# Kernel optimization log

Measured on AMD Instinct MI355X. Metric: run time of the kernel, lower is better.

Reference implementation:

```python
import jax, jax.numpy as jnp
import numpy as np

N_NODES = 50000


def setup_inputs() -> dict:
    key = jax.random.key(0)
    k1, k2, k3, k4 = jax.random.split(key, 4)
    in_c, out_c = 128, 128
    x = jax.random.normal(k1, (N_NODES, in_c), dtype=jnp.float32)
    edge_index = jax.random.randint(k2, (2, 600000), 0, N_NODES, dtype=jnp.int64)
    W_l = jax.random.normal(k3, (out_c, in_c), dtype=jnp.float32) / np.sqrt(in_c)
    W_r = jax.random.normal(k4, (out_c, in_c), dtype=jnp.float32) / np.sqrt(in_c)
    b = jnp.zeros((out_c,), dtype=jnp.float32)
    return {"x": x, "edge_index": edge_index, "W_l": W_l, "W_r": W_r, "b": b}


def reference(x, edge_index, W_l, W_r, b):
    # SAGEConv (PyG defaults): mean aggregation over incoming neighbors,
    # out = lin_l(mean_agg) + lin_r(x) + bias, then log_softmax over features.
    src, dst = edge_index[0], edge_index[1]
    msgs = x[src]  # [E, in_c] gather of source features
    summed = jax.ops.segment_sum(msgs, dst, num_segments=N_NODES)  # [N, in_c]
    counts = jax.ops.segment_sum(jnp.ones_like(dst, dtype=x.dtype), dst,
                                 num_segments=N_NODES)  # [N]
    agg = summed / jnp.maximum(counts, 1.0)[:, None]  # mean; 0 for isolated nodes
    out = agg @ W_l.T + x @ W_r.T + b  # [N, out_c]
    return jax.nn.log_softmax(out, axis=1)
```

## Files before the change

### kernel.cpp

```cpp
#include <hip/hip_runtime.h>
#include <cmath>

#define C    128
#define PAD  64
#define NXCD 8

typedef __bf16 bf16x8 __attribute__((ext_vector_type(8)));
typedef float  f32x4  __attribute__((ext_vector_type(4)));
typedef unsigned short u16x8 __attribute__((ext_vector_type(8)));

static __device__ __forceinline__ unsigned short f2b(float f) {
    unsigned int u = __builtin_bit_cast(unsigned int, f);
    u += 0x7FFFu + ((u >> 16) & 1u);
    return (unsigned short)(u >> 16);
}
static __device__ __forceinline__ float b2f(unsigned short u) {
    return __builtin_bit_cast(float, (unsigned int)u << 16);
}

__global__ __launch_bounds__(256)
void sage_init(const float* __restrict__ Wl, const float* __restrict__ Wr,
               int4* __restrict__ counts4, unsigned short* __restrict__ wp,
               int n4, int ZB) {
    int bid = blockIdx.x;
    int t = threadIdx.x;
    if (bid < ZB) {
        int i = bid * 256 + t;
        if (i < n4) counts4[i] = make_int4(0, 0, 0, 0);
    } else {
        int s = (bid - ZB) * 256 + t;
        int f = s >> 6, l = s & 63;
        int kt = f >> 4, mt = f & 15;
        int g = l >> 4;
        int m = mt * 16 + (l & 15);
        const float* src = (m < C) ? (Wl + (size_t)m * C)
                                   : (Wr + (size_t)(m - C) * C);
        u16x8 o;
#pragma unroll
        for (int j = 0; j < 8; ++j) o[j] = f2b(src[kt * 32 + g * 8 + j]);
        *(u16x8*)(wp + (size_t)s * 8) = o;
    }
}

__global__ __launch_bounds__(256)
void sage_fill_gemm(const float* __restrict__ x,
                    const unsigned short* __restrict__ wp,
                    const float* __restrict__ bias,
                    const int* __restrict__ ei,
                    int* __restrict__ counts, unsigned short* __restrict__ csr,
                    unsigned short* __restrict__ yl,
                    unsigned short* __restrict__ yr,
                    int N, int E, int FB) {
    int bid = blockIdx.x;
    int t = threadIdx.x;

    if (bid < FB) {
        int xcd = bid & (NXCD - 1);
        int chunk = bid >> 3;
        int span = (N + NXCD - 1) / NXCD;
        int lo = xcd * span;
        int hi = min(N, lo + span);
        int e0 = (chunk * 256 + t) * 8;
        if (e0 + 7 < E) {
            int4 d0 = *(const int4*)(ei + E + e0);
            int4 d1 = *(const int4*)(ei + E + e0 + 4);
            int4 s0 = *(const int4*)(ei + e0);
            int4 s1 = *(const int4*)(ei + e0 + 4);
            int dd[8] = {d0.x, d0.y, d0.z, d0.w, d1.x, d1.y, d1.z, d1.w};
            int ss[8] = {s0.x, s0.y, s0.z, s0.w, s1.x, s1.y, s1.z, s1.w};
#pragma unroll
            for (int j = 0; j < 8; ++j) {
                if (dd[j] >= lo && dd[j] < hi) {
                    int k = atomicAdd(&counts[dd[j]], 1);
                    if (k < PAD)
                        csr[(size_t)dd[j] * PAD + k] = (unsigned short)ss[j];
                }
            }
        } else {
            for (int e = e0; e < E; ++e) {
                int dst = ei[E + e];
                if (dst >= lo && dst < hi) {
                    int k = atomicAdd(&counts[dst], 1);
                    if (k < PAD)
                        csr[(size_t)dst * PAD + k] = (unsigned short)ei[e];
                }
            }
        }
        return;
    }

    int w = t >> 6, l = t & 63;
    int g = l >> 4;

    int node = (bid - FB) * 16 + (l & 15);
    if (node >= N) node = N - 1;
    const float4* xv = (const float4*)(x + (size_t)node * C);
    const bf16x8* A = (const bf16x8*)wp;

    f32x4 acc0 = {0.f,0.f,0.f,0.f}, acc1 = {0.f,0.f,0.f,0.f};
    f32x4 acc2 = {0.f,0.f,0.f,0.f}, acc3 = {0.f,0.f,0.f,0.f};

#pragma unroll
    for (int kt = 0; kt < 4; ++kt) {
        float4 xa = xv[kt * 8 + g * 2];
        float4 xc = xv[kt * 8 + g * 2 + 1];
        u16x8 ab;
        ab[0]=f2b(xa.x); ab[1]=f2b(xa.y); ab[2]=f2b(xa.z); ab[3]=f2b(xa.w);
        ab[4]=f2b(xc.x); ab[5]=f2b(xc.y); ab[6]=f2b(xc.z); ab[7]=f2b(xc.w);
        bf16x8 xf = __builtin_bit_cast(bf16x8, ab);
        int c = w * 4;
        bf16x8 a0 = A[(size_t)(kt * 16 + c + 0) * 64 + l];
        bf16x8 a1 = A[(size_t)(kt * 16 + c + 1) * 64 + l];
        bf16x8 a2 = A[(size_t)(kt * 16 + c + 2) * 64 + l];
        bf16x8 a3 = A[(size_t)(kt * 16 + c + 3) * 64 + l];
        acc0 = __builtin_amdgcn_mfma_f32_16x16x32_bf16(a0, xf, acc0, 0,0,0);
        acc1 = __builtin_amdgcn_mfma_f32_16x16x32_bf16(a1, xf, acc1, 0,0,0);
        acc2 = __builtin_amdgcn_mfma_f32_16x16x32_bf16(a2, xf, acc2, 0,0,0);
        acc3 = __builtin_amdgcn_mfma_f32_16x16x32_bf16(a3, xf, acc3, 0,0,0);
    }

    size_t rowoff = (size_t)node * C;
#pragma unroll
    for (int i = 0; i < 4; ++i) {
        f32x4 a = (i == 0) ? acc0 : (i == 1) ? acc1 : (i == 2) ? acc2 : acc3;
        int mt = w * 4 + i;
        float4 bv = (mt >= 8) ? *(const float4*)(bias + (mt - 8) * 16 + g * 4)
                              : make_float4(0.f, 0.f, 0.f, 0.f);
        ushort4 o;
        o.x = f2b(a[0] + bv.x);
        o.y = f2b(a[1] + bv.y);
        o.z = f2b(a[2] + bv.z);
        o.w = f2b(a[3] + bv.w);
        unsigned short* yp = (mt < 8) ? yl : yr;
        *(ushort4*)(yp + rowoff + (mt & 7) * 16 + g * 4) = o;
    }
}

__global__ __launch_bounds__(256)
void sage_final(const unsigned short* __restrict__ yl,
                const unsigned short* __restrict__ yr,
                const int* __restrict__ counts,
                const unsigned short* __restrict__ csr,
                float* __restrict__ out, int N) {
    int wv = threadIdx.x >> 6;
    int node = blockIdx.x * 4 + wv;
    if (node >= N) return;
    int ln = threadIdx.x & 63;
    int q = ln >> 4;
    int fl = ln & 15;

    int deg = counts[node];
    deg = (deg > PAD) ? PAD : deg;
    int p0 = node * PAD;
    int p1 = p0 + deg;

    float a[8];
#pragma unroll
    for (int j = 0; j < 8; ++j) a[j] = 0.f;

    int p = p0 + q;
    for (; p + 12 < p1; p += 16) {
        int s0 = csr[p], s1 = csr[p + 4], s2 = csr[p + 8], s3 = csr[p + 12];
        u16x8 v0 = *(const u16x8*)(yl + (size_t)s0 * C + fl * 8);
        u16x8 v1 = *(const u16x8*)(yl + (size_t)s1 * C + fl * 8);
        u16x8 v2 = *(const u16x8*)(yl + (size_t)s2 * C + fl * 8);
        u16x8 v3 = *(const u16x8*)(yl + (size_t)s3 * C + fl * 8);
#pragma unroll
        for (int j = 0; j < 8; ++j)
            a[j] += (b2f(v0[j]) + b2f(v1[j])) + (b2f(v2[j]) + b2f(v3[j]));
    }
    for (; p + 4 < p1; p += 8) {
        int s0 = csr[p], s1 = csr[p + 4];
        u16x8 v0 = *(const u16x8*)(yl + (size_t)s0 * C + fl * 8);
        u16x8 v1 = *(const u16x8*)(yl + (size_t)s1 * C + fl * 8);
#pragma unroll
        for (int j = 0; j < 8; ++j) a[j] += b2f(v0[j]) + b2f(v1[j]);
    }
    if (p < p1) {
        int s0 = csr[p];
        u16x8 v0 = *(const u16x8*)(yl + (size_t)s0 * C + fl * 8);
#pragma unroll
        for (int j = 0; j < 8; ++j) a[j] += b2f(v0[j]);
    }

#pragma unroll
    for (int j = 0; j < 8; ++j) {
        a[j] += __shfl_xor(a[j], 16);
        a[j] += __shfl_xor(a[j], 32);
    }
    if (q != 0) return;

    float inv = 1.0f / fmaxf((float)deg, 1.0f);
    u16x8 yv = *(const u16x8*)(yr + (size_t)node * C + fl * 8);
#pragma unroll
    for (int j = 0; j < 8; ++j) a[j] = a[j] * inv + b2f(yv[j]);

    float m = a[0];
#pragma unroll
    for (int j = 1; j < 8; ++j) m = fmaxf(m, a[j]);
#pragma unroll
    for (int off = 1; off < 16; off <<= 1)
        m = fmaxf(m, __shfl_xor(m, off));
    float s = 0.f;
#pragma unroll
    for (int j = 0; j < 8; ++j) s += expf(a[j] - m);
#pragma unroll
    for (int off = 1; off < 16; off <<= 1)
        s += __shfl_xor(s, off);
    float ls = m + logf(s);

    float4 o0, o1;
    o0.x = a[0] - ls; o0.y = a[1] - ls; o0.z = a[2] - ls; o0.w = a[3] - ls;
    o1.x = a[4] - ls; o1.y = a[5] - ls; o1.z = a[6] - ls; o1.w = a[7] - ls;
    float4* op = (float4*)(out + (size_t)node * C + fl * 8);
    op[0] = o0;
    op[1] = o1;
}

extern "C" void kernel_launch(void* const* d_in, const int* in_sizes, int n_in,
                              void* d_out, int out_size, void* d_ws, size_t ws_size,
                              hipStream_t stream) {
    const float* x  = (const float*)d_in[0];
    const int*   ei = (const int*)d_in[1];
    const float* Wl = (const float*)d_in[2];
    const float* Wr = (const float*)d_in[3];
    const float* b  = (const float*)d_in[4];
    float* out = (float*)d_out;

    const int N = in_sizes[0] / C;
    const int E = in_sizes[1] / 2;

    int* counts = (int*)d_ws;
    unsigned short* csr = (unsigned short*)(counts + ((N + 3) & ~3));
    unsigned short* yl  = csr + (size_t)N * PAD;
    unsigned short* yr  = yl + (size_t)N * C;
    unsigned short* wp  = yr + (size_t)N * C;

    int n4 = (N + 3) / 4;
    const int ZB = (n4 + 255) / 256;
    const int NCH = (E + 2047) / 2048;
    const int FB = NCH * NXCD;
    const int NT = (N + 15) / 16;

    sage_init<<<ZB + 16, 256, 0, stream>>>(Wl, Wr, (int4*)counts, wp, n4, ZB);
    sage_fill_gemm<<<FB + NT, 256, 0, stream>>>(x, wp, b, ei, counts, csr,
                                                yl, yr, N, E, FB);
    sage_final<<<(N + 3) / 4, 256, 0, stream>>>(yl, yr, counts, csr, out, N);
}
```

Baseline: 97.84 us.

## Interleave fill and GEMM blocks and keep weight fragments across four tiles

The fused fill/GEMM kernel now interleaves three edge-fill blocks with one GEMM block in each group of four, so the scatter and the matrix work share the GPU at the same time instead of running as two separate block ranges. Each GEMM block loads its weight fragments and bias into registers once and reuses them across four 16-node tiles, cutting repeated weight loads and the number of GEMM blocks. This raises register use per thread and serialises four tiles inside one block, which may reduce latency hiding.

```diff
diff --git a/kernel.cpp b/kernel.cpp
--- a/kernel.cpp
+++ b/kernel.cpp
@@ -50,13 +50,17 @@
                     int* __restrict__ counts, unsigned short* __restrict__ csr,
                     unsigned short* __restrict__ yl,
                     unsigned short* __restrict__ yr,
-                    int N, int E, int FB) {
+                    int N, int E, int FB, int NT) {
     int bid = blockIdx.x;
     int t = threadIdx.x;
-
-    if (bid < FB) {
-        int xcd = bid & (NXCD - 1);
-        int chunk = bid >> 3;
+    int grp = bid >> 2;
+    int pos = bid & 3;
+
+    if (pos < 3) {
+        int idx = grp * 3 + pos;
+        if (idx >= FB) return;
+        int xcd = idx & (NXCD - 1);
+        int chunk = idx >> 3;
         int span = (N + NXCD - 1) / NXCD;
         int lo = xcd * span;
         int hi = min(N, lo + span);
@@ -91,48 +95,62 @@
 
     int w = t >> 6, l = t & 63;
     int g = l >> 4;
-
-    int node = (bid - FB) * 16 + (l & 15);
-    if (node >= N) node = N - 1;
-    const float4* xv = (const float4*)(x + (size_t)node * C);
     const bf16x8* A = (const bf16x8*)wp;
 
-    f32x4 acc0 = {0.f,0.f,0.f,0.f}, acc1 = {0.f,0.f,0.f,0.f};
-    f32x4 acc2 = {0.f,0.f,0.f,0.f}, acc3 = {0.f,0.f,0.f,0.f};
-
+    bf16x8 wf0[4], wf1[4], wf2[4], wf3[4];
 #pragma unroll
     for (int kt = 0; kt < 4; ++kt) {
-        float4 xa = xv[kt * 8 + g * 2];
-        float4 xc = xv[kt * 8 + g * 2 + 1];
-        u16x8 ab;
-        ab[0]=f2b(xa.x); ab[1]=f2b(xa.y); ab[2]=f2b(xa.z); ab[3]=f2b(xa.w);
-        ab[4]=f2b(xc.x); ab[5]=f2b(xc.y); ab[6]=f2b(xc.z); ab[7]=f2b(xc.w);
-        bf16x8 xf = __builtin_bit_cast(bf16x8, ab);
-        int c = w * 4;
-        bf16x8 a0 = A[(size_t)(kt * 16 + c + 0) * 64 + l];
-        bf16x8 a1 = A[(size_t)(kt * 16 + c + 1) * 64 + l];
-        bf16x8 a2 = A[(size_t)(kt * 16 + c + 2) * 64 + l];
-        bf16x8 a3 = A[(size_t)(kt * 16 + c + 3) * 64 + l];
-        acc0 = __builtin_amdgcn_mfma_f32_16x16x32_bf16(a0, xf, acc0, 0,0,0);
-        acc1 = __builtin_amdgcn_mfma_f32_16x16x32_bf16(a1, xf, acc1, 0,0,0);
-        acc2 = __builtin_amdgcn_mfma_f32_16x16x32_bf16(a2, xf, acc2, 0,0,0);
-        acc3 = __builtin_amdgcn_mfma_f32_16x16x32_bf16(a3, xf, acc3, 0,0,0);
-    }
-
-    size_t rowoff = (size_t)node * C;
+        wf0[kt] = A[(size_t)(kt * 16 + w * 4 + 0) * 64 + l];
+        wf1[kt] = A[(size_t)(kt * 16 + w * 4 + 1) * 64 + l];
+        wf2[kt] = A[(size_t)(kt * 16 + w * 4 + 2) * 64 + l];
+        wf3[kt] = A[(size_t)(kt * 16 + w * 4 + 3) * 64 + l];
+    }
+    float4 bv[4];
 #pragma unroll
     for (int i = 0; i < 4; ++i) {
-        f32x4 a = (i == 0) ? acc0 : (i == 1) ? acc1 : (i == 2) ? acc2 : acc3;
         int mt = w * 4 + i;
-        float4 bv = (mt >= 8) ? *(const float4*)(bias + (mt - 8) * 16 + g * 4)
-                              : make_float4(0.f, 0.f, 0.f, 0.f);
-        ushort4 o;
-        o.x = f2b(a[0] + bv.x);
-        o.y = f2b(a[1] + bv.y);
-        o.z = f2b(a[2] + bv.z);
-        o.w = f2b(a[3] + bv.w);
-        unsigned short* yp = (mt < 8) ? yl : yr;
-        *(ushort4*)(yp + rowoff + (mt & 7) * 16 + g * 4) = o;
+        bv[i] = (mt >= 8) ? *(const float4*)(bias + (mt - 8) * 16 + g * 4)
+                          : make_float4(0.f, 0.f, 0.f, 0.f);
+    }
+
+#pragma unroll
+    for (int tt = 0; tt < 4; ++tt) {
+        int tile = grp * 4 + tt;
+        if (tile >= NT) break;
+        int node = tile * 16 + (l & 15);
+        if (node >= N) node = N - 1;
+        const float4* xv = (const float4*)(x + (size_t)node * C);
+
+        f32x4 acc0 = {0.f,0.f,0.f,0.f}, acc1 = {0.f,0.f,0.f,0.f};
+        f32x4 acc2 = {0.f,0.f,0.f,0.f}, acc3 = {0.f,0.f,0.f,0.f};
+
+#pragma unroll
+        for (int kt = 0; kt < 4; ++kt) {
+            float4 xa = xv[kt * 8 + g * 2];
+            float4 xc = xv[kt * 8 + g * 2 + 1];
+            u16x8 ab;
+            ab[0]=f2b(xa.x); ab[1]=f2b(xa.y); ab[2]=f2b(xa.z); ab[3]=f2b(xa.w);
+            ab[4]=f2b(xc.x); ab[5]=f2b(xc.y); ab[6]=f2b(xc.z); ab[7]=f2b(xc.w);
+            bf16x8 xf = __builtin_bit_cast(bf16x8, ab);
+            acc0 = __builtin_amdgcn_mfma_f32_16x16x32_bf16(wf0[kt], xf, acc0, 0,0,0);
+            acc1 = __builtin_amdgcn_mfma_f32_16x16x32_bf16(wf1[kt], xf, acc1, 0,0,0);
+            acc2 = __builtin_amdgcn_mfma_f32_16x16x32_bf16(wf2[kt], xf, acc2, 0,0,0);
+            acc3 = __builtin_amdgcn_mfma_f32_16x16x32_bf16(wf3[kt], xf, acc3, 0,0,0);
+        }
+
+        size_t rowoff = (size_t)node * C;
+#pragma unroll
+        for (int i = 0; i < 4; ++i) {
+            f32x4 a = (i == 0) ? acc0 : (i == 1) ? acc1 : (i == 2) ? acc2 : acc3;
+            int mt = w * 4 + i;
+            ushort4 o;
+            o.x = f2b(a[0] + bv[i].x);
+            o.y = f2b(a[1] + bv[i].y);
+            o.z = f2b(a[2] + bv[i].z);
+            o.w = f2b(a[3] + bv[i].w);
+            unsigned short* yp = (mt < 8) ? yl : yr;
+            *(ushort4*)(yp + rowoff + (mt & 7) * 16 + g * 4) = o;
+        }
     }
 }
 
@@ -241,9 +259,11 @@
     const int NCH = (E + 2047) / 2048;
     const int FB = NCH * NXCD;
     const int NT = (N + 15) / 16;
+    const int GB = (NT + 3) / 4;
+    const int NGRP = (GB > (FB + 2) / 3) ? GB : (FB + 2) / 3;
 
     sage_init<<<ZB + 16, 256, 0, stream>>>(Wl, Wr, (int4*)counts, wp, n4, ZB);
-    sage_fill_gemm<<<FB + NT, 256, 0, stream>>>(x, wp, b, ei, counts, csr,
-                                                yl, yr, N, E, FB);
+    sage_fill_gemm<<<NGRP * 4, 256, 0, stream>>>(x, wp, b, ei, counts, csr,
+                                                 yl, yr, N, E, FB, NT);
     sage_final<<<(N + 3) / 4, 256, 0, stream>>>(yl, yr, counts, csr, out, N);
 }
```

New measurement: 111.6 us. 1.14x slower.

## Interleave edge-fill blocks with GEMM tiles and drop XCD-partitioned edge replay

Applied to the files above, without the earlier changes.

Edge-fill blocks previously ran as 8 XCD-partitioned passes, each rereading every edge and keeping only destinations in its node span so that atomics stayed local to one XCD. Now each edge chunk is read once by a single block, and these blocks are interleaved one in every 11 with GEMM tile blocks so the atomic-heavy fill overlaps the compute. This cuts edge-index reads eightfold and balances the two kinds of work across the grid. The cost is that counter atomics now hit lines shared across XCDs, which may add coherence traffic.

```diff
diff --git a/kernel.cpp b/kernel.cpp
--- a/kernel.cpp
+++ b/kernel.cpp
@@ -3,7 +3,6 @@
 
 #define C    128
 #define PAD  64
-#define NXCD 8
 
 typedef __bf16 bf16x8 __attribute__((ext_vector_type(8)));
 typedef float  f32x4  __attribute__((ext_vector_type(4)));
@@ -50,17 +49,16 @@
                     int* __restrict__ counts, unsigned short* __restrict__ csr,
                     unsigned short* __restrict__ yl,
                     unsigned short* __restrict__ yr,
-                    int N, int E, int FB) {
+                    int N, int E, int FB, int NT) {
     int bid = blockIdx.x;
     int t = threadIdx.x;
-
-    if (bid < FB) {
-        int xcd = bid & (NXCD - 1);
-        int chunk = bid >> 3;
-        int span = (N + NXCD - 1) / NXCD;
-        int lo = xcd * span;
-        int hi = min(N, lo + span);
-        int e0 = (chunk * 256 + t) * 8;
+    int grp = bid / 11;
+    int pos = bid % 11;
+
+    if (pos == 0) {
+        int idx = grp;
+        if (idx >= FB) return;
+        int e0 = (idx * 256 + t) * 8;
         if (e0 + 7 < E) {
             int4 d0 = *(const int4*)(ei + E + e0);
             int4 d1 = *(const int4*)(ei + E + e0 + 4);
@@ -70,29 +68,28 @@
             int ss[8] = {s0.x, s0.y, s0.z, s0.w, s1.x, s1.y, s1.z, s1.w};
 #pragma unroll
             for (int j = 0; j < 8; ++j) {
-                if (dd[j] >= lo && dd[j] < hi) {
-                    int k = atomicAdd(&counts[dd[j]], 1);
-                    if (k < PAD)
-                        csr[(size_t)dd[j] * PAD + k] = (unsigned short)ss[j];
-                }
+                int k = atomicAdd(&counts[dd[j]], 1);
+                if (k < PAD)
+                    csr[(size_t)dd[j] * PAD + k] = (unsigned short)ss[j];
             }
         } else {
             for (int e = e0; e < E; ++e) {
                 int dst = ei[E + e];
-                if (dst >= lo && dst < hi) {
-                    int k = atomicAdd(&counts[dst], 1);
-                    if (k < PAD)
-                        csr[(size_t)dst * PAD + k] = (unsigned short)ei[e];
-                }
+                int k = atomicAdd(&counts[dst], 1);
+                if (k < PAD)
+                    csr[(size_t)dst * PAD + k] = (unsigned short)ei[e];
             }
         }
         return;
     }
 
+    int tile = grp * 10 + (pos - 1);
+    if (tile >= NT) return;
+
     int w = t >> 6, l = t & 63;
     int g = l >> 4;
 
-    int node = (bid - FB) * 16 + (l & 15);
+    int node = tile * 16 + (l & 15);
     if (node >= N) node = N - 1;
     const float4* xv = (const float4*)(x + (size_t)node * C);
     const bf16x8* A = (const bf16x8*)wp;
@@ -238,12 +235,14 @@
 
     int n4 = (N + 3) / 4;
     const int ZB = (n4 + 255) / 256;
-    const int NCH = (E + 2047) / 2048;
-    const int FB = NCH * NXCD;
+    const int FB = (E + 2047) / 2048;
     const int NT = (N + 15) / 16;
+    const int NG1 = FB;
+    const int NG10 = (NT + 9) / 10;
+    const int NGRP = (NG1 > NG10) ? NG1 : NG10;
 
     sage_init<<<ZB + 16, 256, 0, stream>>>(Wl, Wr, (int4*)counts, wp, n4, ZB);
-    sage_fill_gemm<<<FB + NT, 256, 0, stream>>>(x, wp, b, ei, counts, csr,
-                                                yl, yr, N, E, FB);
+    sage_fill_gemm<<<NGRP * 11, 256, 0, stream>>>(x, wp, b, ei, counts, csr,
+                                                  yl, yr, N, E, FB, NT);
     sage_final<<<(N + 3) / 4, 256, 0, stream>>>(yl, yr, counts, csr, out, N);
 }
```

After: 85.20 us. -12.9%, faster.
